# Kernel optimization log

Hardware: AMD Instinct MI355X
Metric: run time of the kernel (lower is better)

Reference implementation:

```python
import jax, jax.numpy as jnp
import numpy as np

N_NODES = 50000
N_EDGES = 800000
DIM_IN = 64
DIM_HID = 128
DIM_OUT = 64


def _linear_init(key, fan_in, fan_out):
    # torch nn.Linear default: U(-1/sqrt(fan_in), 1/sqrt(fan_in)) for W and b
    kw, kb = jax.random.split(key)
    bound = 1.0 / np.sqrt(fan_in)
    W = jax.random.uniform(kw, (fan_in, fan_out), minval=-bound, maxval=bound, dtype=jnp.float32)
    b = jax.random.uniform(kb, (fan_out,), minval=-bound, maxval=bound, dtype=jnp.float32)
    return W, b


def setup_inputs() -> dict:
    key = jax.random.key(0)
    kx, ke, k0, k1, k2 = jax.random.split(key, 5)
    x = jax.random.normal(kx, (N_NODES, DIM_IN), dtype=jnp.float32)
    edge_idx = jax.random.randint(ke, (2, N_EDGES), 0, N_NODES, dtype=jnp.int64)
    W0, b0 = _linear_init(k0, 2 * DIM_IN, DIM_HID)
    W1, b1 = _linear_init(k1, DIM_HID, DIM_HID)
    W2, b2 = _linear_init(k2, DIM_HID, DIM_OUT)
    return {"x": x, "edge_idx": edge_idx, "W0": W0, "b0": b0,
            "W1": W1, "b1": b1, "W2": W2, "b2": b2}


def reference(x, edge_idx, W0, b0, W1, b1, W2, b2):
    row, col = edge_idx[0], edge_idx[1]
    # gather + concat edge features: [E, 2*dim_in]
    h = jnp.concatenate([x[row], x[col]], axis=-1)
    h = jax.nn.softplus(h @ W0 + b0)
    h = jax.nn.softplus(h @ W1 + b1)
    h = h @ W2 + b2  # [E, dim_out]
    # scatter-add edge messages to source nodes
    return jax.ops.segment_sum(h, row, num_segments=x.shape[0])
```

## Files before the change

### kernel.cpp

```cpp
#include <hip/hip_runtime.h>
#include <math.h>

#define N_NODES 50000
#define N_EDGES 800000
#define DIM_IN 64
#define DIM_HID 128
#define DIM_OUT 64
#define PAD 136

typedef __attribute__((ext_vector_type(8))) short short8;
typedef __attribute__((ext_vector_type(4))) float f32x4;

union U8 { uint4 u; short8 s; };

__device__ __forceinline__ unsigned short f2bf(float f) {
    unsigned u = __float_as_uint(f);
    return (unsigned short)((u + 0x7fffu + ((u >> 16) & 1u)) >> 16);
}

__device__ __forceinline__ unsigned cvt_pk_bf16(float a, float b) {
#if __has_builtin(__builtin_amdgcn_cvt_pk_bf16_f32)
    auto pk = __builtin_amdgcn_cvt_pk_bf16_f32(a, b);
    unsigned d; __builtin_memcpy(&d, &pk, 4);
    return d;
#else
    return (unsigned)f2bf(a) | ((unsigned)f2bf(b) << 16);
#endif
}

__device__ __forceinline__ float exp2_fast(float a) {
#if __has_builtin(__builtin_amdgcn_exp2f)
    return __builtin_amdgcn_exp2f(a);
#else
    return __expf(a * 0.69314718f);
#endif
}

__device__ __forceinline__ unsigned sp2(float x0, float x1) {
    const float L2E = 1.44269504f;
    float z0 = exp2_fast(-fabsf(x0) * L2E);
    float z1 = exp2_fast(-fabsf(x1) * L2E);
    float p0 = fmaf(fmaf(fmaf(-0.1011458f, z0, 0.2942925f), z0, -0.5f), z0, 1.0f) * z0;
    float p1 = fmaf(fmaf(fmaf(-0.1011458f, z1, 0.2942925f), z1, -0.5f), z1, 1.0f) * z1;
    return cvt_pk_bf16(fmaxf(x0, 0.0f) + p0, fmaxf(x1, 0.0f) + p1);
}

__global__ void prep_weights(const float* __restrict__ W0,
                             const float* __restrict__ W1,
                             const float* __restrict__ W2,
                             unsigned short* __restrict__ wt) {
    int i = blockIdx.x * blockDim.x + threadIdx.x;
    if (i >= 320 * PAD) return;
    int row = i / PAD, s = i - row * PAD;
    float v = 0.f;
    if (s < 128) {
        int f = ((s >> 5) << 5) | (((s & 7) >> 2) << 4) | (((s >> 3) & 3) << 2) | (s & 3);
        if (row < 128)      v = W0[s * DIM_HID + row];
        else if (row < 256) v = W1[f * DIM_HID + (row - 128)];
        else                v = W2[f * DIM_OUT + (row - 256)];
    }
    wt[i] = f2bf(v);
}

__global__ __launch_bounds__(256, 4)
void edge_mlp_mfma(const float* __restrict__ x,
                   const int* __restrict__ eidx,
                   const unsigned short* __restrict__ wt,
                   const float* __restrict__ b0,
                   const float* __restrict__ b1,
                   const float* __restrict__ b2,
                   float* __restrict__ out) {
    const int lane = threadIdx.x & 63;
    const int w    = threadIdx.x >> 6;
    const int l16  = lane & 15;
    const int q    = lane >> 4;
    const int e0w  = blockIdx.x * 128 + w * 32;

    const unsigned short* Wt0 = wt;
    const unsigned short* Wt1 = wt + 128 * PAD;
    const unsigned short* Wt2 = wt + 256 * PAD;

    int nodeR[2], nodeC[2];
#pragma unroll
    for (int m = 0; m < 2; ++m) {
        nodeR[m] = eidx[e0w + m * 16 + l16];
        nodeC[m] = eidx[N_EDGES + e0w + m * 16 + l16];
    }

    short8 hfr[2][4];
#pragma unroll
    for (int m = 0; m < 2; ++m)
#pragma unroll
        for (int kk = 0; kk < 4; ++kk) {
            int node = (kk >= 2) ? nodeC[m] : nodeR[m];
            const float* p = x + (size_t)node * DIM_IN + (kk & 1) * 32 + q * 8;
            float4 v0 = *(const float4*)p;
            float4 v1 = *(const float4*)(p + 4);
            U8 t;
            t.u.x = cvt_pk_bf16(v0.x, v0.y);
            t.u.y = cvt_pk_bf16(v0.z, v0.w);
            t.u.z = cvt_pk_bf16(v1.x, v1.y);
            t.u.w = cvt_pk_bf16(v1.z, v1.w);
            hfr[m][kk] = t.s;
        }

#pragma unroll
    for (int L = 0; L < 2; ++L) {
        const unsigned short* W = L ? Wt1 : Wt0;
        const float* bias = L ? b1 : b0;
        unsigned d[2][8][2];
#pragma unroll
        for (int ti = 0; ti < 8; ++ti) {
            f32x4 bb = *(const f32x4*)(bias + ti * 16 + q * 4);
            f32x4 a0 = bb, a1 = bb;
            const unsigned short* Wp = W + (ti * 16 + l16) * PAD + q * 8;
            short8 wf[4];
#pragma unroll
            for (int kk = 0; kk < 4; ++kk)
                wf[kk] = *(const short8*)(Wp + kk * 32);
#pragma unroll
            for (int kk = 0; kk < 4; ++kk) {
                a0 = __builtin_amdgcn_mfma_f32_16x16x32_bf16(wf[kk], hfr[0][kk], a0, 0, 0, 0);
                a1 = __builtin_amdgcn_mfma_f32_16x16x32_bf16(wf[kk], hfr[1][kk], a1, 0, 0, 0);
            }
            d[0][ti][0] = sp2(a0[0], a0[1]);
            d[0][ti][1] = sp2(a0[2], a0[3]);
            d[1][ti][0] = sp2(a1[0], a1[1]);
            d[1][ti][1] = sp2(a1[2], a1[3]);
        }
#pragma unroll
        for (int m = 0; m < 2; ++m)
#pragma unroll
            for (int kk = 0; kk < 4; ++kk) {
                U8 t;
                t.u.x = d[m][2 * kk][0];
                t.u.y = d[m][2 * kk][1];
                t.u.z = d[m][2 * kk + 1][0];
                t.u.w = d[m][2 * kk + 1][1];
                hfr[m][kk] = t.s;
            }
    }

    int nodeO[2][4];
#pragma unroll
    for (int m = 0; m < 2; ++m)
#pragma unroll
        for (int r = 0; r < 4; ++r)
            nodeO[m][r] = eidx[e0w + m * 16 + q * 4 + r];

#pragma unroll
    for (int ti = 0; ti < 4; ++ti) {
        float bv = b2[ti * 16 + l16];
        f32x4 a0 = (f32x4){bv, bv, bv, bv};
        f32x4 a1 = a0;
        const unsigned short* Wp = Wt2 + (ti * 16 + l16) * PAD + q * 8;
        short8 wf[4];
#pragma unroll
        for (int kk = 0; kk < 4; ++kk)
            wf[kk] = *(const short8*)(Wp + kk * 32);
#pragma unroll
        for (int kk = 0; kk < 4; ++kk) {
            a0 = __builtin_amdgcn_mfma_f32_16x16x32_bf16(hfr[0][kk], wf[kk], a0, 0, 0, 0);
            a1 = __builtin_amdgcn_mfma_f32_16x16x32_bf16(hfr[1][kk], wf[kk], a1, 0, 0, 0);
        }
#pragma unroll
        for (int r = 0; r < 4; ++r) {
            atomicAdd(out + (size_t)nodeO[0][r] * DIM_OUT + ti * 16 + l16, a0[r]);
            atomicAdd(out + (size_t)nodeO[1][r] * DIM_OUT + ti * 16 + l16, a1[r]);
        }
    }
}

extern "C" void kernel_launch(void* const* d_in, const int* in_sizes, int n_in,
                              void* d_out, int out_size, void* d_ws, size_t ws_size,
                              hipStream_t stream) {
    const float* x  = (const float*)d_in[0];
    const int*   ei = (const int*)d_in[1];
    const float* W0 = (const float*)d_in[2];
    const float* b0 = (const float*)d_in[3];
    const float* W1 = (const float*)d_in[4];
    const float* b1 = (const float*)d_in[5];
    const float* W2 = (const float*)d_in[6];
    const float* b2 = (const float*)d_in[7];
    float* out = (float*)d_out;
    unsigned short* wt = (unsigned short*)d_ws;

    hipMemsetAsync(out, 0, (size_t)N_NODES * DIM_OUT * sizeof(float), stream);

    const int wn = 320 * PAD;
    prep_weights<<<(wn + 255) / 256, 256, 0, stream>>>(W0, W1, W2, wt);

    edge_mlp_mfma<<<N_EDGES / 128, 256, 0, stream>>>(x, ei, wt, b0, b1, b2, out);
}
```

Measured before the change: 294.8 us.

## Bucket edges by destination node block and accumulate scatter in LDS

A new pre-pass kernel buckets edge ids by groups of 49 destination nodes, using one global atomic counter per group. The main kernel then runs one block per group and scatter-adds edge messages into a shared-memory accumulator, followed by a plain vectorized store. This removes the full output memset and the many per-element global float atomics. In exchange it adds an extra kernel with contended counter atomics and an extra indirection per edge. Edges beyond the per-bucket capacity would be silently dropped, and the old atomic path is kept as a fallback when workspace is too small.

```diff
diff --git a/kernel.cpp b/kernel.cpp
--- a/kernel.cpp
+++ b/kernel.cpp
@@ -7,6 +7,13 @@
 #define DIM_HID 128
 #define DIM_OUT 64
 #define PAD 136
+
+#define NPB  49
+#define NB   1021
+#define ACCS 68
+
+#define WS_OFF_CNT 87040
+#define WS_OFF_LST 152576
 
 typedef __attribute__((ext_vector_type(8))) short short8;
 typedef __attribute__((ext_vector_type(4))) float f32x4;
@@ -62,14 +69,168 @@
     wt[i] = f2bf(v);
 }
 
+__global__ void bucket_kernel(const int* __restrict__ eidx,
+                              int* __restrict__ cnts,
+                              int* __restrict__ lists, int CAP) {
+    int e = blockIdx.x * 256 + threadIdx.x;
+    if (e >= N_EDGES) return;
+    int row = eidx[e];
+    int b = row / NPB;
+    int slot = atomicAdd(&cnts[b * 16], 1);
+    if (slot < CAP) lists[(size_t)b * CAP + slot] = e;
+}
+
 __global__ __launch_bounds__(256, 4)
-void edge_mlp_mfma(const float* __restrict__ x,
-                   const int* __restrict__ eidx,
-                   const unsigned short* __restrict__ wt,
-                   const float* __restrict__ b0,
-                   const float* __restrict__ b1,
-                   const float* __restrict__ b2,
-                   float* __restrict__ out) {
+void edge_mlp_bucket(const float* __restrict__ x,
+                     const int* __restrict__ eidx,
+                     const unsigned short* __restrict__ wt,
+                     const float* __restrict__ b0,
+                     const float* __restrict__ b1,
+                     const float* __restrict__ b2,
+                     const int* __restrict__ cnts,
+                     const int* __restrict__ lists, int CAP,
+                     float* __restrict__ out) {
+    __shared__ __align__(16) float acc[NPB * ACCS];
+
+    const int tid  = threadIdx.x;
+    const int base = blockIdx.x * NPB;
+    const int nn   = min(NPB, N_NODES - base);
+
+    for (int i = tid; i < NPB * ACCS; i += 256) acc[i] = 0.f;
+    __syncthreads();
+
+    const int cnt = min(cnts[blockIdx.x * 16], CAP);
+    const int* lst = lists + (size_t)blockIdx.x * CAP;
+
+    const int lane = tid & 63;
+    const int w    = tid >> 6;
+    const int l16  = lane & 15;
+    const int q    = lane >> 4;
+
+    const unsigned short* Wt0 = wt;
+    const unsigned short* Wt1 = wt + 128 * PAD;
+    const unsigned short* Wt2 = wt + 256 * PAD;
+
+    for (int i0 = w * 32; i0 < cnt; i0 += 4 * 32) {
+        int eI[2];
+#pragma unroll
+        for (int m = 0; m < 2; ++m)
+            eI[m] = lst[min(i0 + m * 16 + l16, cnt - 1)];
+
+        int nodeR[2], nodeC[2];
+#pragma unroll
+        for (int m = 0; m < 2; ++m) {
+            nodeR[m] = eidx[eI[m]];
+            nodeC[m] = eidx[N_EDGES + eI[m]];
+        }
+
+        short8 hfr[2][4];
+#pragma unroll
+        for (int m = 0; m < 2; ++m)
+#pragma unroll
+            for (int kk = 0; kk < 4; ++kk) {
+                int node = (kk >= 2) ? nodeC[m] : nodeR[m];
+                const float* p = x + (size_t)node * DIM_IN + (kk & 1) * 32 + q * 8;
+                float4 v0 = *(const float4*)p;
+                float4 v1 = *(const float4*)(p + 4);
+                U8 t;
+                t.u.x = cvt_pk_bf16(v0.x, v0.y);
+                t.u.y = cvt_pk_bf16(v0.z, v0.w);
+                t.u.z = cvt_pk_bf16(v1.x, v1.y);
+                t.u.w = cvt_pk_bf16(v1.z, v1.w);
+                hfr[m][kk] = t.s;
+            }
+
+#pragma unroll
+        for (int L = 0; L < 2; ++L) {
+            const unsigned short* W = L ? Wt1 : Wt0;
+            const float* bias = L ? b1 : b0;
+            unsigned d[2][8][2];
+#pragma unroll
+            for (int ti = 0; ti < 8; ++ti) {
+                f32x4 bb = *(const f32x4*)(bias + ti * 16 + q * 4);
+                f32x4 a0 = bb, a1 = bb;
+                const unsigned short* Wp = W + (ti * 16 + l16) * PAD + q * 8;
+                short8 wf[4];
+#pragma unroll
+                for (int kk = 0; kk < 4; ++kk)
+                    wf[kk] = *(const short8*)(Wp + kk * 32);
+#pragma unroll
+                for (int kk = 0; kk < 4; ++kk) {
+                    a0 = __builtin_amdgcn_mfma_f32_16x16x32_bf16(wf[kk], hfr[0][kk], a0, 0, 0, 0);
+                    a1 = __builtin_amdgcn_mfma_f32_16x16x32_bf16(wf[kk], hfr[1][kk], a1, 0, 0, 0);
+                }
+                d[0][ti][0] = sp2(a0[0], a0[1]);
+                d[0][ti][1] = sp2(a0[2], a0[3]);
+                d[1][ti][0] = sp2(a1[0], a1[1]);
+                d[1][ti][1] = sp2(a1[2], a1[3]);
+            }
+#pragma unroll
+            for (int m = 0; m < 2; ++m)
+#pragma unroll
+                for (int kk = 0; kk < 4; ++kk) {
+                    U8 t;
+                    t.u.x = d[m][2 * kk][0];
+                    t.u.y = d[m][2 * kk][1];
+                    t.u.z = d[m][2 * kk + 1][0];
+                    t.u.w = d[m][2 * kk + 1][1];
+                    hfr[m][kk] = t.s;
+                }
+        }
+
+        int nl[2][4];
+        bool gv[2][4];
+#pragma unroll
+        for (int m = 0; m < 2; ++m)
+#pragma unroll
+            for (int r = 0; r < 4; ++r) {
+                int pos = i0 + m * 16 + q * 4 + r;
+                bool v = pos < cnt;
+                gv[m][r] = v;
+                int e = lst[v ? pos : 0];
+                nl[m][r] = v ? (eidx[e] - base) : 0;
+            }
+
+#pragma unroll
+        for (int ti = 0; ti < 4; ++ti) {
+            float bv = b2[ti * 16 + l16];
+            f32x4 a0 = (f32x4){bv, bv, bv, bv};
+            f32x4 a1 = a0;
+            const unsigned short* Wp = Wt2 + (ti * 16 + l16) * PAD + q * 8;
+            short8 wf[4];
+#pragma unroll
+            for (int kk = 0; kk < 4; ++kk)
+                wf[kk] = *(const short8*)(Wp + kk * 32);
+#pragma unroll
+            for (int kk = 0; kk < 4; ++kk) {
+                a0 = __builtin_amdgcn_mfma_f32_16x16x32_bf16(hfr[0][kk], wf[kk], a0, 0, 0, 0);
+                a1 = __builtin_amdgcn_mfma_f32_16x16x32_bf16(hfr[1][kk], wf[kk], a1, 0, 0, 0);
+            }
+#pragma unroll
+            for (int r = 0; r < 4; ++r) {
+                if (gv[0][r]) atomicAdd(&acc[nl[0][r] * ACCS + ti * 16 + l16], a0[r]);
+                if (gv[1][r]) atomicAdd(&acc[nl[1][r] * ACCS + ti * 16 + l16], a1[r]);
+            }
+        }
+    }
+
+    __syncthreads();
+    const float4* accv = (const float4*)acc;
+    float4* outv = (float4*)out;
+    for (int i = tid; i < nn * 16; i += 256) {
+        int nlw = i >> 4, fq = i & 15;
+        outv[(size_t)(base + nlw) * 16 + fq] = accv[nlw * 17 + fq];
+    }
+}
+
+__global__ __launch_bounds__(256, 4)
+void edge_mlp_atomic(const float* __restrict__ x,
+                     const int* __restrict__ eidx,
+                     const unsigned short* __restrict__ wt,
+                     const float* __restrict__ b0,
+                     const float* __restrict__ b1,
+                     const float* __restrict__ b2,
+                     float* __restrict__ out) {
     const int lane = threadIdx.x & 63;
     const int w    = threadIdx.x >> 6;
     const int l16  = lane & 15;
@@ -183,12 +344,25 @@
     const float* W2 = (const float*)d_in[6];
     const float* b2 = (const float*)d_in[7];
     float* out = (float*)d_out;
+
     unsigned short* wt = (unsigned short*)d_ws;
-
-    hipMemsetAsync(out, 0, (size_t)N_NODES * DIM_OUT * sizeof(float), stream);
+    int* cnts  = (int*)((char*)d_ws + WS_OFF_CNT);
+    int* lists = (int*)((char*)d_ws + WS_OFF_LST);
 
     const int wn = 320 * PAD;
     prep_weights<<<(wn + 255) / 256, 256, 0, stream>>>(W0, W1, W2, wt);
 
-    edge_mlp_mfma<<<N_EDGES / 128, 256, 0, stream>>>(x, ei, wt, b0, b1, b2, out);
-}
+    long avail = (long)ws_size - (long)WS_OFF_LST;
+    int CAP = (avail > 0) ? (int)(avail / ((long)NB * 4)) : 0;
+    if (CAP > 3072) CAP = 3072;
+
+    if (CAP >= 1280) {
+        hipMemsetAsync(cnts, 0, NB * 16 * sizeof(int), stream);
+        bucket_kernel<<<(N_EDGES + 255) / 256, 256, 0, stream>>>(ei, cnts, lists, CAP);
+        edge_mlp_bucket<<<NB, 256, 0, stream>>>(x, ei, wt, b0, b1, b2,
+                                                cnts, lists, CAP, out);
+    } else {
+        hipMemsetAsync(out, 0, (size_t)N_NODES * DIM_OUT * sizeof(float), stream);
+        edge_mlp_atomic<<<N_EDGES / 128, 256, 0, stream>>>(x, ei, wt, b0, b1, b2, out);
+    }
+}
```

Result: slower. 840.0 us (+184.9%).

## Fuse memset, weight prep and edge MLP into one persistent cooperative kernel

Applied to the files above, without the earlier changes.

Replaces the memset, the weight-prep kernel and the edge MLP kernel with one cooperative persistent kernel. The kernel zeroes the output and converts the weights, then does a grid-wide sync and loops over edge tiles. It also drops the PAD row stride in favour of a 128 stride and loads weight fragments inside the MFMA loop. The aim is to remove launch gaps and per-block startup cost, but the grid sync and grid-stride tiling add serialisation, and the unpadded stride may cause cache-set conflicts.

```diff
diff --git a/kernel.cpp b/kernel.cpp
--- a/kernel.cpp
+++ b/kernel.cpp
@@ -1,4 +1,5 @@
 #include <hip/hip_runtime.h>
+#include <hip/hip_cooperative_groups.h>
 #include <math.h>
 
 #define N_NODES 50000
@@ -6,7 +7,7 @@
 #define DIM_IN 64
 #define DIM_HID 128
 #define DIM_OUT 64
-#define PAD 136
+#define NTILES 6250
 
 typedef __attribute__((ext_vector_type(8))) short short8;
 typedef __attribute__((ext_vector_type(4))) float f32x4;
@@ -45,128 +46,129 @@
     return cvt_pk_bf16(fmaxf(x0, 0.0f) + p0, fmaxf(x1, 0.0f) + p1);
 }
 
-__global__ void prep_weights(const float* __restrict__ W0,
-                             const float* __restrict__ W1,
-                             const float* __restrict__ W2,
-                             unsigned short* __restrict__ wt) {
-    int i = blockIdx.x * blockDim.x + threadIdx.x;
-    if (i >= 320 * PAD) return;
-    int row = i / PAD, s = i - row * PAD;
-    float v = 0.f;
-    if (s < 128) {
+__global__ __launch_bounds__(256, 4)
+void fused_mlp(const float* __restrict__ x,
+               const int* __restrict__ eidx,
+               const float* __restrict__ W0, const float* __restrict__ b0,
+               const float* __restrict__ W1, const float* __restrict__ b1,
+               const float* __restrict__ W2, const float* __restrict__ b2,
+               unsigned short* __restrict__ wt,
+               float* __restrict__ out) {
+    const int gtid = blockIdx.x * 256 + threadIdx.x;
+    const int T = gridDim.x * 256;
+
+    float4 z4 = make_float4(0.f, 0.f, 0.f, 0.f);
+    float4* o4 = (float4*)out;
+    for (int i = gtid; i < (N_NODES * DIM_OUT) / 4; i += T) o4[i] = z4;
+
+    for (int i = gtid; i < 320 * 128; i += T) {
+        int row = i >> 7, s = i & 127;
         int f = ((s >> 5) << 5) | (((s & 7) >> 2) << 4) | (((s >> 3) & 3) << 2) | (s & 3);
+        float v;
         if (row < 128)      v = W0[s * DIM_HID + row];
         else if (row < 256) v = W1[f * DIM_HID + (row - 128)];
         else                v = W2[f * DIM_OUT + (row - 256)];
+        wt[i] = f2bf(v);
     }
-    wt[i] = f2bf(v);
-}
-
-__global__ __launch_bounds__(256, 4)
-void edge_mlp_mfma(const float* __restrict__ x,
-                   const int* __restrict__ eidx,
-                   const unsigned short* __restrict__ wt,
-                   const float* __restrict__ b0,
-                   const float* __restrict__ b1,
-                   const float* __restrict__ b2,
-                   float* __restrict__ out) {
+
+    __threadfence();
+    cooperative_groups::this_grid().sync();
+
     const int lane = threadIdx.x & 63;
     const int w    = threadIdx.x >> 6;
     const int l16  = lane & 15;
     const int q    = lane >> 4;
-    const int e0w  = blockIdx.x * 128 + w * 32;
 
     const unsigned short* Wt0 = wt;
-    const unsigned short* Wt1 = wt + 128 * PAD;
-    const unsigned short* Wt2 = wt + 256 * PAD;
-
-    int nodeR[2], nodeC[2];
-#pragma unroll
-    for (int m = 0; m < 2; ++m) {
-        nodeR[m] = eidx[e0w + m * 16 + l16];
-        nodeC[m] = eidx[N_EDGES + e0w + m * 16 + l16];
-    }
-
-    short8 hfr[2][4];
-#pragma unroll
-    for (int m = 0; m < 2; ++m)
-#pragma unroll
-        for (int kk = 0; kk < 4; ++kk) {
-            int node = (kk >= 2) ? nodeC[m] : nodeR[m];
-            const float* p = x + (size_t)node * DIM_IN + (kk & 1) * 32 + q * 8;
-            float4 v0 = *(const float4*)p;
-            float4 v1 = *(const float4*)(p + 4);
-            U8 t;
-            t.u.x = cvt_pk_bf16(v0.x, v0.y);
-            t.u.y = cvt_pk_bf16(v0.z, v0.w);
-            t.u.z = cvt_pk_bf16(v1.x, v1.y);
-            t.u.w = cvt_pk_bf16(v1.z, v1.w);
-            hfr[m][kk] = t.s;
+    const unsigned short* Wt1 = wt + 128 * 128;
+    const unsigned short* Wt2 = wt + 256 * 128;
+
+#pragma unroll 1
+    for (int tile = blockIdx.x; tile < NTILES; tile += gridDim.x) {
+        const int e0w = tile * 128 + w * 32;
+
+        int nodeR[2], nodeC[2];
+#pragma unroll
+        for (int m = 0; m < 2; ++m) {
+            nodeR[m] = eidx[e0w + m * 16 + l16];
+            nodeC[m] = eidx[N_EDGES + e0w + m * 16 + l16];
         }
 
-#pragma unroll
-    for (int L = 0; L < 2; ++L) {
-        const unsigned short* W = L ? Wt1 : Wt0;
-        const float* bias = L ? b1 : b0;
-        unsigned d[2][8][2];
-#pragma unroll
-        for (int ti = 0; ti < 8; ++ti) {
-            f32x4 bb = *(const f32x4*)(bias + ti * 16 + q * 4);
-            f32x4 a0 = bb, a1 = bb;
-            const unsigned short* Wp = W + (ti * 16 + l16) * PAD + q * 8;
-            short8 wf[4];
-#pragma unroll
-            for (int kk = 0; kk < 4; ++kk)
-                wf[kk] = *(const short8*)(Wp + kk * 32);
+        short8 hfr[2][4];
+#pragma unroll
+        for (int m = 0; m < 2; ++m)
 #pragma unroll
             for (int kk = 0; kk < 4; ++kk) {
-                a0 = __builtin_amdgcn_mfma_f32_16x16x32_bf16(wf[kk], hfr[0][kk], a0, 0, 0, 0);
-                a1 = __builtin_amdgcn_mfma_f32_16x16x32_bf16(wf[kk], hfr[1][kk], a1, 0, 0, 0);
-            }
-            d[0][ti][0] = sp2(a0[0], a0[1]);
-            d[0][ti][1] = sp2(a0[2], a0[3]);
-            d[1][ti][0] = sp2(a1[0], a1[1]);
-            d[1][ti][1] = sp2(a1[2], a1[3]);
+                int node = (kk >= 2) ? nodeC[m] : nodeR[m];
+                const float* p = x + ((size_t)node << 6) + ((kk & 1) << 5) + (q << 3);
+                float4 v0 = *(const float4*)p;
+                float4 v1 = *(const float4*)(p + 4);
+                U8 t;
+                t.u.x = cvt_pk_bf16(v0.x, v0.y);
+                t.u.y = cvt_pk_bf16(v0.z, v0.w);
+                t.u.z = cvt_pk_bf16(v1.x, v1.y);
+                t.u.w = cvt_pk_bf16(v1.z, v1.w);
+                hfr[m][kk] = t.s;
+            }
+
+#pragma unroll
+        for (int L = 0; L < 2; ++L) {
+            const unsigned short* W = L ? Wt1 : Wt0;
+            const float* bias = L ? b1 : b0;
+            unsigned d[2][8][2];
+#pragma unroll
+            for (int ti = 0; ti < 8; ++ti) {
+                f32x4 bb = *(const f32x4*)(bias + ti * 16 + q * 4);
+                f32x4 a0 = bb, a1 = bb;
+                const unsigned short* Wp = W + ((ti * 16 + l16) << 7) + q * 8;
+#pragma unroll
+                for (int kk = 0; kk < 4; ++kk) {
+                    short8 wf = *(const short8*)(Wp + kk * 32);
+                    a0 = __builtin_amdgcn_mfma_f32_16x16x32_bf16(wf, hfr[0][kk], a0, 0, 0, 0);
+                    a1 = __builtin_amdgcn_mfma_f32_16x16x32_bf16(wf, hfr[1][kk], a1, 0, 0, 0);
+                }
+                d[0][ti][0] = sp2(a0[0], a0[1]);
+                d[0][ti][1] = sp2(a0[2], a0[3]);
+                d[1][ti][0] = sp2(a1[0], a1[1]);
+                d[1][ti][1] = sp2(a1[2], a1[3]);
+            }
+#pragma unroll
+            for (int m = 0; m < 2; ++m)
+#pragma unroll
+                for (int kk = 0; kk < 4; ++kk) {
+                    U8 t;
+                    t.u.x = d[m][2 * kk][0];
+                    t.u.y = d[m][2 * kk][1];
+                    t.u.z = d[m][2 * kk + 1][0];
+                    t.u.w = d[m][2 * kk + 1][1];
+                    hfr[m][kk] = t.s;
+                }
         }
+
+        int nodeO[2][4];
 #pragma unroll
         for (int m = 0; m < 2; ++m)
 #pragma unroll
+            for (int r = 0; r < 4; ++r)
+                nodeO[m][r] = eidx[e0w + m * 16 + q * 4 + r];
+
+#pragma unroll
+        for (int ti = 0; ti < 4; ++ti) {
+            float bv = b2[ti * 16 + l16];
+            f32x4 a0 = (f32x4){bv, bv, bv, bv};
+            f32x4 a1 = a0;
+            const unsigned short* Wp = Wt2 + ((ti * 16 + l16) << 7) + q * 8;
+#pragma unroll
             for (int kk = 0; kk < 4; ++kk) {
-                U8 t;
-                t.u.x = d[m][2 * kk][0];
-                t.u.y = d[m][2 * kk][1];
-                t.u.z = d[m][2 * kk + 1][0];
-                t.u.w = d[m][2 * kk + 1][1];
-                hfr[m][kk] = t.s;
-            }
-    }
-
-    int nodeO[2][4];
-#pragma unroll
-    for (int m = 0; m < 2; ++m)
-#pragma unroll
-        for (int r = 0; r < 4; ++r)
-            nodeO[m][r] = eidx[e0w + m * 16 + q * 4 + r];
-
-#pragma unroll
-    for (int ti = 0; ti < 4; ++ti) {
-        float bv = b2[ti * 16 + l16];
-        f32x4 a0 = (f32x4){bv, bv, bv, bv};
-        f32x4 a1 = a0;
-        const unsigned short* Wp = Wt2 + (ti * 16 + l16) * PAD + q * 8;
-        short8 wf[4];
-#pragma unroll
-        for (int kk = 0; kk < 4; ++kk)
-            wf[kk] = *(const short8*)(Wp + kk * 32);
-#pragma unroll
-        for (int kk = 0; kk < 4; ++kk) {
-            a0 = __builtin_amdgcn_mfma_f32_16x16x32_bf16(hfr[0][kk], wf[kk], a0, 0, 0, 0);
-            a1 = __builtin_amdgcn_mfma_f32_16x16x32_bf16(hfr[1][kk], wf[kk], a1, 0, 0, 0);
-        }
-#pragma unroll
-        for (int r = 0; r < 4; ++r) {
-            atomicAdd(out + (size_t)nodeO[0][r] * DIM_OUT + ti * 16 + l16, a0[r]);
-            atomicAdd(out + (size_t)nodeO[1][r] * DIM_OUT + ti * 16 + l16, a1[r]);
+                short8 wf = *(const short8*)(Wp + kk * 32);
+                a0 = __builtin_amdgcn_mfma_f32_16x16x32_bf16(hfr[0][kk], wf, a0, 0, 0, 0);
+                a1 = __builtin_amdgcn_mfma_f32_16x16x32_bf16(hfr[1][kk], wf, a1, 0, 0, 0);
+            }
+#pragma unroll
+            for (int r = 0; r < 4; ++r) {
+                atomicAdd(out + ((size_t)nodeO[0][r] << 6) + ti * 16 + l16, a0[r]);
+                atomicAdd(out + ((size_t)nodeO[1][r] << 6) + ti * 16 + l16, a1[r]);
+            }
         }
     }
 }
@@ -185,10 +187,15 @@
     float* out = (float*)d_out;
     unsigned short* wt = (unsigned short*)d_ws;
 
-    hipMemsetAsync(out, 0, (size_t)N_NODES * DIM_OUT * sizeof(float), stream);
-
-    const int wn = 320 * PAD;
-    prep_weights<<<(wn + 255) / 256, 256, 0, stream>>>(W0, W1, W2, wt);
-
-    edge_mlp_mfma<<<N_EDGES / 128, 256, 0, stream>>>(x, ei, wt, b0, b1, b2, out);
-}
+    int maxb = 0;
+    hipOccupancyMaxActiveBlocksPerMultiprocessor(&maxb, (const void*)fused_mlp, 256, 0);
+    if (maxb < 1) maxb = 1;
+    if (maxb > 8) maxb = 8;
+    int grid = maxb * 256;
+
+    void* args[] = {(void*)&x, (void*)&ei,
+                    (void*)&W0, (void*)&b0, (void*)&W1, (void*)&b1,
+                    (void*)&W2, (void*)&b2, (void*)&wt, (void*)&out};
+    hipLaunchCooperativeKernel((const void*)fused_mlp, dim3(grid), dim3(256),
+                               args, 0, stream);
+}
```

New measurement: 758.0 us. 157% more time.
